# Performance work log

Hardware: AMD Instinct MI355X
Metric: run time of the kernel (lower is better)

Reference implementation:

```python
import jax, jax.numpy as jnp
import numpy as np

B = 32768
SEQ_LEN = 24
H = 64            # HIDDEN_DIM
SLOTS = 8         # MEMORY_SLOTS
VOCAB = 64        # VOCAB_SIZE


def setup_inputs() -> dict:
    key = jax.random.key(0)
    ks = jax.random.split(key, 8)
    seqs = jax.random.randint(ks[0], (B, SEQ_LEN), 0, VOCAB, dtype=jnp.int64)
    query_tok = jax.random.randint(ks[1], (B,), 0, VOCAB + 2, dtype=jnp.int64)
    embed = jax.random.normal(ks[2], (VOCAB + 2, H), dtype=jnp.float32) * 0.05
    gw1 = jax.random.normal(ks[3], (2 * H, 32), dtype=jnp.float32) / np.sqrt(2 * H)
    gb1 = jnp.zeros((32,), jnp.float32)
    gw2 = jax.random.normal(ks[4], (32, 1), dtype=jnp.float32) / np.sqrt(32)
    gb2 = jnp.zeros((1,), jnp.float32)
    rw1 = jax.random.normal(ks[5], (2 * H, H), dtype=jnp.float32) / np.sqrt(2 * H)
    rb1 = jnp.zeros((H,), jnp.float32)
    rw2 = jax.random.normal(ks[6], (H, VOCAB), dtype=jnp.float32) / np.sqrt(H)
    rb2 = jnp.zeros((VOCAB,), jnp.float32)
    return {"seqs": seqs, "query_tok": query_tok, "embed": embed,
            "gw1": gw1, "gb1": gb1, "gw2": gw2, "gb2": gb2,
            "rw1": rw1, "rb1": rb1, "rw2": rw2, "rb2": rb2}


def reference(seqs, query_tok, embed, gw1, gb1, gw2, gb2, rw1, rb1, rw2, rb2):
    Bb = seqs.shape[0]
    T = SEQ_LEN - 1  # model writes tokens 0..SEQ_LEN-2 into memory
    embs = embed[seqs[:, :T]]                     # [B, T, H]
    batch_idx = jnp.arange(Bb)

    def step(mem, xs):
        t, emb = xs                               # emb: [B, H]
        ctx = jnp.broadcast_to(emb[:, None, :], mem.shape)
        pair = jnp.concatenate([ctx, mem], axis=-1)        # [B, S, 2H]
        h = jax.nn.relu(pair @ gw1 + gb1)                  # [B, S, 32]
        score = jax.nn.sigmoid(h @ gw2 + gb2)[..., 0]      # [B, S]
        # while memory not full, fill slot t; otherwise evict argmax score
        idx = jnp.where(t < SLOTS, t, jnp.argmax(score, axis=1))
        mem = mem.at[batch_idx, idx].set(emb)
        return mem, None

    mem0 = jnp.zeros((Bb, SLOTS, H), embed.dtype)
    mem, _ = jax.lax.scan(step, mem0, (jnp.arange(T), jnp.swapaxes(embs, 0, 1)))

    summary = mem.mean(axis=1)                    # [B, H]  (memory is full: T > SLOTS)
    q = embed[query_tok]                          # [B, H]
    x = jnp.concatenate([q, summary], axis=-1)    # [B, 2H]
    logits = jax.nn.relu(x @ rw1 + rb1) @ rw2 + rb2   # [B, VOCAB]
    return logits
```

## Files before the change

kernel.cpp:

```cpp
#include <hip/hip_runtime.h>
#include <math.h>

typedef __attribute__((ext_vector_type(8))) _Float16 f16x8;
typedef __attribute__((ext_vector_type(4))) float f32x4;

#define TSTEPS 23
#define ROWS 128

#define WSB_B1 0
#define WSB_W2 21504
#define WSB_Z  30720

__global__ __launch_bounds__(512) void pre_all(
    const float* __restrict__ embed, const float* __restrict__ gw1,
    const float* __restrict__ gb1, const float* __restrict__ gw2,
    const float* __restrict__ gb2, const float* __restrict__ rw1,
    const float* __restrict__ rb1, const float* __restrict__ rw2,
    char* __restrict__ wsc)
{
    __shared__ float sEmb[66 * 64];
    __shared__ float sW[128 * 64];
    __shared__ float sV[64 * 33];
    __shared__ float sU[32];
    __shared__ float sG[65];
    __shared__ float sRb1[64];
    __shared__ double sP[512];

    const int tid = threadIdx.x;
    const int blk = blockIdx.x;

    if (blk < 64) {
        {
            const float4* es = (const float4*)embed;
            float4* ed = (float4*)sEmb;
            for (int i = tid; i < 1024; i += 512) ed[i] = es[i];
            const float4* gs = (const float4*)gw1;
            float4* gd = (float4*)sW;
            for (int i = tid; i < 1024; i += 512) gd[i] = gs[i];
            if (tid < 32) { sG[tid] = gb1[tid]; sG[32 + tid] = gw2[tid]; }
            if (tid == 64) sG[64] = gb2[0];
        }
        __syncthreads();
        {
            const int s = tid >> 3, j0 = (tid & 7) * 4;
            const float* er = sEmb + s * 64;
            float a0 = 0.f, a1 = 0.f, a2 = 0.f, a3 = 0.f;
            #pragma unroll
            for (int k = 0; k < 64; ++k) {
                const float ek = er[k];
                const float4 w0 = *(const float4*)&sW[(64 + k) * 32 + j0];
                a0 = fmaf(ek, w0.x, a0); a1 = fmaf(ek, w0.y, a1);
                a2 = fmaf(ek, w0.z, a2); a3 = fmaf(ek, w0.w, a3);
            }
            float* vd = sV + s * 33 + j0;
            vd[0] = a0; vd[1] = a1; vd[2] = a2; vd[3] = a3;
        }
        if (tid < 32) {
            const int j = tid;
            float acc = 0.f;
            const float* er = sEmb + blk * 64;
            #pragma unroll
            for (int k = 0; k < 64; ++k)
                acc = fmaf(er[k], sW[k * 32 + j], acc);
            sU[j] = acc;
        }
        __syncthreads();
        {
            const int s = tid >> 3;
            const int j0 = (tid & 7) * 4;
            double p = 0.0;
            #pragma unroll
            for (int j = j0; j < j0 + 4; ++j) {
                const double a = (double)sU[j] + (double)sV[s * 33 + j] + (double)sG[j];
                if (a > 0.0) p += a * (double)sG[32 + j];
            }
            sP[tid] = p;
        }
        __syncthreads();
        if (tid < 64) {
            const double* pp = sP + tid * 8;
            const double z = (double)sG[64] +
                (((pp[0] + pp[1]) + (pp[2] + pp[3])) + ((pp[4] + pp[5]) + (pp[6] + pp[7])));
            ((float*)(wsc + WSB_Z))[blk * 64 + tid] = (float)z;
        }
    } else if (blk < 81) {
        {
            const float4* es = (const float4*)embed;
            float4* ed = (float4*)sEmb;
            for (int i = tid; i < 1056; i += 512) ed[i] = es[i];
            const float4* rs = (const float4*)rw1;
            float4* rd = (float4*)sW;
            for (int i = tid; i < 2048; i += 512) rd[i] = rs[i];
            if (tid < 64) sRb1[tid] = rb1[tid];
        }
        __syncthreads();
        const int e = (blk - 64) * 512 + tid;
        if (e < 8320) {
            const int n = e & 63, k = e >> 6;
            const int trow = (k < 64) ? k : (k - 64);
            const int ofs = (k < 64) ? 64 : 0;
            float4 er[16];
            const float4* erp = (const float4*)(sEmb + trow * 64);
            #pragma unroll
            for (int q = 0; q < 16; ++q) er[q] = erp[q];
            float acc = (k < 64) ? 0.f : sRb1[n];
            #pragma unroll
            for (int m = 0; m < 64; ++m)
                acc = fmaf(((const float*)er)[m], sW[(ofs + m) * 64 + n], acc);
            acc *= (k < 64) ? (0.125f * 256.f) : 256.f;
            ((_Float16*)(wsc + WSB_B1))[n * 168 + k] = (_Float16)acc;
        }
    } else {
        _Float16* w2t = (_Float16*)(wsc + WSB_W2);
        for (int e = tid; e < 4096; e += 512) {
            const int n = e & 63, j = e >> 6;
            w2t[n * 72 + j] = (_Float16)rw2[j * 64 + n];
        }
        _Float16* b1 = (_Float16*)(wsc + WSB_B1);
        for (int e = tid; e < 2432; e += 512) {
            const int n = e / 38, k = 130 + (e - n * 38);
            b1[n * 168 + k] = (_Float16)0.f;
        }
    }
}

__device__ __forceinline__ f16x8 build_slot_win(const unsigned* s, const unsigned* hb, int ko)
{
    unsigned w0 = 0, w1 = 0, w2 = 0, w3 = 0;
    #pragma unroll
    for (int i = 0; i < 8; ++i) {
        const unsigned d = s[i] - (unsigned)ko;
        const unsigned val = (d < 8u) ? (hb[i] << ((d & 1u) * 16)) : 0u;
        const unsigned q = d >> 1;
        w0 |= (q == 0u) ? val : 0u;
        w1 |= (q == 1u) ? val : 0u;
        w2 |= (q == 2u) ? val : 0u;
        w3 |= (q == 3u) ? val : 0u;
    }
    union { unsigned u[4]; f16x8 v; } r;
    r.u[0] = w0; r.u[1] = w1; r.u[2] = w2; r.u[3] = w3;
    return r.v;
}

__device__ __forceinline__ f16x8 build_q_win(int kq, int ko)
{
    const unsigned d = (unsigned)(kq - ko);
    const unsigned val = (d < 8u) ? (0x3C00u << ((d & 1u) * 16)) : 0u;
    const unsigned q = d >> 1;
    union { unsigned u[4]; f16x8 v; } r;
    r.u[0] = (q == 0u) ? val : 0u;
    r.u[1] = (q == 1u) ? val : 0u;
    r.u[2] = (q == 2u) ? val : 0u;
    r.u[3] = (q == 3u) ? val : 0u;
    return r.v;
}

#define L_Z    0
#define L_B1   16640
#define L_W2   38144
#define L_H    47360
#define L_ROW  65792
#define L_RB2  67840

__global__ __launch_bounds__(512) void sm_main(
    const int* __restrict__ seqs, const int* __restrict__ qtok,
    const float* __restrict__ rb2, const char* __restrict__ wsc,
    float* __restrict__ out)
{
    __shared__ __align__(16) char smem[68096];
    float*    sZ   = (float*)(smem + L_Z);
    _Float16* sB1  = (_Float16*)(smem + L_B1);
    _Float16* sW2  = (_Float16*)(smem + L_W2);
    _Float16* sH   = (_Float16*)(smem + L_H);
    uint4*    sRow = (uint4*)(smem + L_ROW);
    float*    sRb2 = (float*)(smem + L_RB2);

    const int tid = threadIdx.x;
    const int base = blockIdx.x * ROWS;

    unsigned pk[6];
    int qt = 0;
    if (tid < ROWS) {
        const int4* sq = (const int4*)(seqs + (size_t)(base + tid) * 24);
        #pragma unroll
        for (int i = 0; i < 6; ++i) {
            const int4 w4 = sq[i];
            pk[i] = (unsigned)w4.x | ((unsigned)w4.y << 8) |
                    ((unsigned)w4.z << 16) | ((unsigned)w4.w << 24);
        }
        qt = qtok[base + tid];
    }

    {
        const float* zsrc = (const float*)(wsc + WSB_Z);
        #pragma unroll
        for (int i = 0; i < 8; ++i) {
            const int e = tid + i * 512;
            sZ[(e >> 6) * 65 + (e & 63)] = zsrc[e];
        }
        if (tid < 64) sRb2[tid] = rb2[tid];
    }
    __syncthreads();

    if (tid < ROWS) {
        unsigned lo = pk[0], hi = pk[1];
        #pragma unroll
        for (int t = 8; t < TSTEPS; ++t) {
            const int c = (int)((pk[t >> 2] >> ((t & 3) * 8)) & 255u);
            const float* zr = sZ + c * 65;
            float b = zr[lo & 63]; int am = 0; float z;
            z = zr[(lo >> 8) & 63];  if (z > b) { b = z; am = 1; }
            z = zr[(lo >> 16) & 63]; if (z > b) { b = z; am = 2; }
            z = zr[lo >> 24];        if (z > b) { b = z; am = 3; }
            z = zr[hi & 63];         if (z > b) { b = z; am = 4; }
            z = zr[(hi >> 8) & 63];  if (z > b) { b = z; am = 5; }
            z = zr[(hi >> 16) & 63]; if (z > b) { b = z; am = 6; }
            z = zr[hi >> 24];        if (z > b) { b = z; am = 7; }
            const unsigned cb = (unsigned)c;
            if (am < 4) { const int sh = am * 8; lo = (lo & ~(255u << sh)) | (cb << sh); }
            else        { const int sh = am * 8 - 32; hi = (hi & ~(255u << sh)) | (cb << sh); }
        }
        int t_[8] = { (int)(lo & 63), (int)((lo >> 8) & 63), (int)((lo >> 16) & 63), (int)(lo >> 24),
                      (int)(hi & 63), (int)((hi >> 8) & 63), (int)((hi >> 16) & 63), (int)(hi >> 24) };
        int tot[8] = {1, 1, 1, 1, 1, 1, 1, 1};
        #pragma unroll
        for (int i = 0; i < 8; ++i)
            #pragma unroll
            for (int j = i + 1; j < 8; ++j) {
                const int eq = (t_[i] == t_[j]);
                tot[i] += eq; tot[j] += eq;
            }
        unsigned tp = 0;
        #pragma unroll
        for (int i = 0; i < 8; ++i) tp |= (unsigned)tot[i] << (4 * i);
        sRow[tid] = make_uint4(lo & 0x3F3F3F3Fu, hi & 0x3F3F3F3Fu, tp, (unsigned)qt);
    } else {
        const int t2 = tid - 128;
        const float4* b1s = (const float4*)(wsc + WSB_B1);
        float4* b1d = (float4*)sB1;
        for (int i = t2; i < 1344; i += 384) b1d[i] = b1s[i];
        const float4* w2s = (const float4*)(wsc + WSB_W2);
        float4* w2d = (float4*)sW2;
        for (int i = t2; i < 576; i += 384) w2d[i] = w2s[i];
    }
    __syncthreads();

    const int lane = tid & 63;
    const int w = tid >> 6;
    const int c16 = lane & 15, g = lane >> 4;
    const int arow = w * 16 + c16;

    unsigned sl[8], hb[8];
    int kq;
    {
        const uint4 ri = sRow[arow];
        sl[0] = ri.x & 63u; sl[1] = (ri.x >> 8) & 63u;
        sl[2] = (ri.x >> 16) & 63u; sl[3] = ri.x >> 24;
        sl[4] = ri.y & 63u; sl[5] = (ri.y >> 8) & 63u;
        sl[6] = (ri.y >> 16) & 63u; sl[7] = ri.y >> 24;
        #pragma unroll
        for (int i = 0; i < 8; ++i) {
            const unsigned tot = (ri.z >> (4 * i)) & 15u;
            union { _Float16 h; unsigned short b; } cv;
            cv.h = (_Float16)(float)tot;
            hb[i] = (unsigned)cv.b;
        }
        kq = 64 + (int)ri.w;
    }

    f32x4 a0 = {0.f, 0.f, 0.f, 0.f}, a1 = a0, a2 = a0, a3 = a0;
    #pragma unroll
    for (int ks = 0; ks < 5; ++ks) {
        const int ko = ks * 32 + g * 8;
        const f16x8 af = (ks < 2) ? build_slot_win(sl, hb, ko) : build_q_win(kq, ko);
        const f16x8 b0 = *(const f16x8*)&sB1[(c16) * 168 + ko];
        const f16x8 b1 = *(const f16x8*)&sB1[(16 + c16) * 168 + ko];
        const f16x8 b2 = *(const f16x8*)&sB1[(32 + c16) * 168 + ko];
        const f16x8 b3 = *(const f16x8*)&sB1[(48 + c16) * 168 + ko];
        a0 = __builtin_amdgcn_mfma_f32_16x16x32_f16(af, b0, a0, 0, 0, 0);
        a1 = __builtin_amdgcn_mfma_f32_16x16x32_f16(af, b1, a1, 0, 0, 0);
        a2 = __builtin_amdgcn_mfma_f32_16x16x32_f16(af, b2, a2, 0, 0, 0);
        a3 = __builtin_amdgcn_mfma_f32_16x16x32_f16(af, b3, a3, 0, 0, 0);
    }
    {
        const int rbase = w * 16 + g * 4;
        #pragma unroll
        for (int j = 0; j < 4; ++j) {
            _Float16* hr = sH + (rbase + j) * 72;
            const float v0 = a0[j], v1 = a1[j], v2 = a2[j], v3 = a3[j];
            hr[c16]      = (_Float16)(v0 > 0.f ? v0 : 0.f);
            hr[16 + c16] = (_Float16)(v1 > 0.f ? v1 : 0.f);
            hr[32 + c16] = (_Float16)(v2 > 0.f ? v2 : 0.f);
            hr[48 + c16] = (_Float16)(v3 > 0.f ? v3 : 0.f);
        }
    }
    __syncthreads();

    f32x4 d0 = {0.f, 0.f, 0.f, 0.f}, d1 = d0, d2 = d0, d3 = d0;
    #pragma unroll
    for (int ks = 0; ks < 2; ++ks) {
        const int ko = ks * 32 + g * 8;
        const f16x8 af = *(const f16x8*)&sH[arow * 72 + ko];
        const f16x8 b0 = *(const f16x8*)&sW2[(c16) * 72 + ko];
        const f16x8 b1 = *(const f16x8*)&sW2[(16 + c16) * 72 + ko];
        const f16x8 b2 = *(const f16x8*)&sW2[(32 + c16) * 72 + ko];
        const f16x8 b3 = *(const f16x8*)&sW2[(48 + c16) * 72 + ko];
        d0 = __builtin_amdgcn_mfma_f32_16x16x32_f16(af, b0, d0, 0, 0, 0);
        d1 = __builtin_amdgcn_mfma_f32_16x16x32_f16(af, b1, d1, 0, 0, 0);
        d2 = __builtin_amdgcn_mfma_f32_16x16x32_f16(af, b2, d2, 0, 0, 0);
        d3 = __builtin_amdgcn_mfma_f32_16x16x32_f16(af, b3, d3, 0, 0, 0);
    }
    float* sOut = (float*)(void*)smem;
    {
        const int rbase = w * 16 + g * 4;
        #pragma unroll
        for (int j = 0; j < 4; ++j) {
            float* orow = sOut + (rbase + j) * 68;
            orow[c16]      = d0[j] * (1.f / 256.f) + sRb2[c16];
            orow[16 + c16] = d1[j] * (1.f / 256.f) + sRb2[16 + c16];
            orow[32 + c16] = d2[j] * (1.f / 256.f) + sRb2[32 + c16];
            orow[48 + c16] = d3[j] * (1.f / 256.f) + sRb2[48 + c16];
        }
    }
    __syncthreads();

    #pragma unroll
    for (int r2 = 0; r2 < 4; ++r2) {
        const int idx = r2 * 512 + tid;
        const int row = idx >> 4, c4 = idx & 15;
        *(float4*)(out + (size_t)(base + row) * 64 + c4 * 4) =
            *(const float4*)&sOut[row * 68 + c4 * 4];
    }
}

extern "C" void kernel_launch(void* const* d_in, const int* in_sizes, int n_in,
                              void* d_out, int out_size, void* d_ws, size_t ws_size,
                              hipStream_t stream)
{
    const int* seqs    = (const int*)d_in[0];
    const int* qtok    = (const int*)d_in[1];
    const float* embed = (const float*)d_in[2];
    const float* gw1   = (const float*)d_in[3];
    const float* gb1   = (const float*)d_in[4];
    const float* gw2   = (const float*)d_in[5];
    const float* gb2   = (const float*)d_in[6];
    const float* rw1   = (const float*)d_in[7];
    const float* rb1   = (const float*)d_in[8];
    const float* rw2   = (const float*)d_in[9];
    const float* rb2   = (const float*)d_in[10];
    char* wsc  = (char*)d_ws;
    float* out = (float*)d_out;
    const int B = in_sizes[1];

    pre_all<<<82, 512, 0, stream>>>(embed, gw1, gb1, gw2, gb2, rw1, rb1, rw2, wsc);
    pre_all<<<64, 512, 0, stream>>>(embed, gw1, gb1, gw2, gb2, rw1, rb1, rw2, wsc);
    sm_main<<<B / ROWS, 512, 0, stream>>>(seqs, qtok, rb2, wsc, out);
}
```

Measured before the change: 23.14 us.

## Split eviction scan across 4 lanes per row, halve block size, drop duplicate prelaunch

After: 22.72 us. About the same (-1.8%).

```diff
diff --git a/kernel.cpp b/kernel.cpp
--- a/kernel.cpp
+++ b/kernel.cpp
@@ -5,7 +5,8 @@
 typedef __attribute__((ext_vector_type(4))) float f32x4;
 
 #define TSTEPS 23
-#define ROWS 128
+#define ROWS 64
+#define BT 256
 
 #define WSB_B1 0
 #define WSB_W2 21504
@@ -159,89 +160,99 @@
 #define L_B1   16640
 #define L_W2   38144
 #define L_H    47360
-#define L_ROW  65792
-#define L_RB2  67840
-
-__global__ __launch_bounds__(512) void sm_main(
+#define L_TOK  56576
+#define L_ROW  58112
+#define L_QT   59136
+
+__global__ __launch_bounds__(BT) void sm_main(
     const int* __restrict__ seqs, const int* __restrict__ qtok,
     const float* __restrict__ rb2, const char* __restrict__ wsc,
     float* __restrict__ out)
 {
-    __shared__ __align__(16) char smem[68096];
+    __shared__ __align__(16) char smem[59648];
     float*    sZ   = (float*)(smem + L_Z);
     _Float16* sB1  = (_Float16*)(smem + L_B1);
     _Float16* sW2  = (_Float16*)(smem + L_W2);
     _Float16* sH   = (_Float16*)(smem + L_H);
-    uint4*    sRow = (uint4*)(smem + L_ROW);
-    float*    sRb2 = (float*)(smem + L_RB2);
+    unsigned* sTok = (unsigned*)(smem + L_TOK);
+    uint4*    sRow = (uint4*)(smem + 58112);
+    int*      sQt  = (int*)(smem + 59136);
+    float*    sRb2 = (float*)(smem + 59392);
 
     const int tid = threadIdx.x;
     const int base = blockIdx.x * ROWS;
 
-    unsigned pk[6];
-    int qt = 0;
-    if (tid < ROWS) {
-        const int4* sq = (const int4*)(seqs + (size_t)(base + tid) * 24);
-        #pragma unroll
-        for (int i = 0; i < 6; ++i) {
-            const int4 w4 = sq[i];
-            pk[i] = (unsigned)w4.x | ((unsigned)w4.y << 8) |
-                    ((unsigned)w4.z << 16) | ((unsigned)w4.w << 24);
-        }
-        qt = qtok[base + tid];
-    }
-
-    {
+    {
+        const int4* sq = (const int4*)(seqs + (size_t)base * 24);
+        #pragma unroll
+        for (int i = 0; i < 2; ++i) {
+            const int g = tid + i * 256;
+            if (g < 384) {
+                const int4 w4 = sq[g];
+                sTok[g] = (unsigned)w4.x | ((unsigned)w4.y << 8) |
+                          ((unsigned)w4.z << 16) | ((unsigned)w4.w << 24);
+            }
+        }
+        if (tid < 64) sQt[tid] = qtok[base + tid];
+        if (tid >= 64 && tid < 128) sRb2[tid - 64] = rb2[tid - 64];
         const float* zsrc = (const float*)(wsc + WSB_Z);
         #pragma unroll
-        for (int i = 0; i < 8; ++i) {
-            const int e = tid + i * 512;
+        for (int i = 0; i < 16; ++i) {
+            const int e = tid + i * 256;
             sZ[(e >> 6) * 65 + (e & 63)] = zsrc[e];
         }
-        if (tid < 64) sRb2[tid] = rb2[tid];
-    }
-    __syncthreads();
-
-    if (tid < ROWS) {
-        unsigned lo = pk[0], hi = pk[1];
-        #pragma unroll
-        for (int t = 8; t < TSTEPS; ++t) {
-            const int c = (int)((pk[t >> 2] >> ((t & 3) * 8)) & 255u);
-            const float* zr = sZ + c * 65;
-            float b = zr[lo & 63]; int am = 0; float z;
-            z = zr[(lo >> 8) & 63];  if (z > b) { b = z; am = 1; }
-            z = zr[(lo >> 16) & 63]; if (z > b) { b = z; am = 2; }
-            z = zr[lo >> 24];        if (z > b) { b = z; am = 3; }
-            z = zr[hi & 63];         if (z > b) { b = z; am = 4; }
-            z = zr[(hi >> 8) & 63];  if (z > b) { b = z; am = 5; }
-            z = zr[(hi >> 16) & 63]; if (z > b) { b = z; am = 6; }
-            z = zr[hi >> 24];        if (z > b) { b = z; am = 7; }
-            const unsigned cb = (unsigned)c;
-            if (am < 4) { const int sh = am * 8; lo = (lo & ~(255u << sh)) | (cb << sh); }
-            else        { const int sh = am * 8 - 32; hi = (hi & ~(255u << sh)) | (cb << sh); }
-        }
-        int t_[8] = { (int)(lo & 63), (int)((lo >> 8) & 63), (int)((lo >> 16) & 63), (int)(lo >> 24),
-                      (int)(hi & 63), (int)((hi >> 8) & 63), (int)((hi >> 16) & 63), (int)(hi >> 24) };
-        int tot[8] = {1, 1, 1, 1, 1, 1, 1, 1};
-        #pragma unroll
-        for (int i = 0; i < 8; ++i)
-            #pragma unroll
-            for (int j = i + 1; j < 8; ++j) {
-                const int eq = (t_[i] == t_[j]);
-                tot[i] += eq; tot[j] += eq;
-            }
-        unsigned tp = 0;
-        #pragma unroll
-        for (int i = 0; i < 8; ++i) tp |= (unsigned)tot[i] << (4 * i);
-        sRow[tid] = make_uint4(lo & 0x3F3F3F3Fu, hi & 0x3F3F3F3Fu, tp, (unsigned)qt);
-    } else {
-        const int t2 = tid - 128;
         const float4* b1s = (const float4*)(wsc + WSB_B1);
         float4* b1d = (float4*)sB1;
-        for (int i = t2; i < 1344; i += 384) b1d[i] = b1s[i];
+        for (int i = tid; i < 1344; i += 256) b1d[i] = b1s[i];
         const float4* w2s = (const float4*)(wsc + WSB_W2);
         float4* w2d = (float4*)sW2;
-        for (int i = t2; i < 576; i += 384) w2d[i] = w2s[i];
+        for (int i = tid; i < 576; i += 256) w2d[i] = w2s[i];
+    }
+    __syncthreads();
+
+    {
+        const int row = tid >> 2, sub = tid & 3;
+        unsigned lo = sTok[row * 6 + 0];
+        unsigned hi = sTok[row * 6 + 1];
+        const unsigned char* tk = ((const unsigned char*)sTok) + row * 24;
+        const int s0 = sub * 2, s1 = sub * 2 + 1;
+        #pragma unroll
+        for (int t = 8; t < TSTEPS; ++t) {
+            const int c = tk[t];
+            const float* zr = sZ + c * 65;
+            const unsigned word = (sub < 2) ? lo : hi;
+            const int sh = (sub & 1) * 16;
+            const int b0 = (int)((word >> sh) & 63u);
+            const int b1 = (int)((word >> (sh + 8)) & 63u);
+            const float v0 = zr[b0], v1 = zr[b1];
+            float bv; int bi;
+            if (v1 > v0) { bv = v1; bi = s1; } else { bv = v0; bi = s0; }
+            #pragma unroll
+            for (int m = 1; m <= 2; m <<= 1) {
+                const float ov = __shfl_xor(bv, m);
+                const int   oi = __shfl_xor(bi, m);
+                if (ov > bv || (ov == bv && oi < bi)) { bv = ov; bi = oi; }
+            }
+            const unsigned cb = (unsigned)c;
+            if (bi < 4) { const int q = bi * 8;      lo = (lo & ~(255u << q)) | (cb << q); }
+            else        { const int q = bi * 8 - 32; hi = (hi & ~(255u << q)) | (cb << q); }
+        }
+        if (sub == 0) {
+            int t_[8] = { (int)(lo & 63), (int)((lo >> 8) & 63), (int)((lo >> 16) & 63), (int)(lo >> 24),
+                          (int)(hi & 63), (int)((hi >> 8) & 63), (int)((hi >> 16) & 63), (int)(hi >> 24) };
+            int tot[8] = {1, 1, 1, 1, 1, 1, 1, 1};
+            #pragma unroll
+            for (int i = 0; i < 8; ++i)
+                #pragma unroll
+                for (int j = i + 1; j < 8; ++j) {
+                    const int eq = (t_[i] == t_[j]);
+                    tot[i] += eq; tot[j] += eq;
+                }
+            unsigned tp = 0;
+            #pragma unroll
+            for (int i = 0; i < 8; ++i) tp |= (unsigned)tot[i] << (4 * i);
+            sRow[row] = make_uint4(lo & 0x3F3F3F3Fu, hi & 0x3F3F3F3Fu, tp, (unsigned)sQt[row]);
+        }
     }
     __syncthreads();
 
@@ -326,7 +337,7 @@
 
     #pragma unroll
     for (int r2 = 0; r2 < 4; ++r2) {
-        const int idx = r2 * 512 + tid;
+        const int idx = r2 * 256 + tid;
         const int row = idx >> 4, c4 = idx & 15;
         *(float4*)(out + (size_t)(base + row) * 64 + c4 * 4) =
             *(const float4*)&sOut[row * 68 + c4 * 4];
@@ -353,6 +364,5 @@
     const int B = in_sizes[1];
 
     pre_all<<<82, 512, 0, stream>>>(embed, gw1, gb1, gw2, gb2, rw1, rb1, rw2, wsc);
-    pre_all<<<64, 512, 0, stream>>>(embed, gw1, gb1, gw2, gb2, rw1, rb1, rw2, wsc);
-    sm_main<<<B / ROWS, 512, 0, stream>>>(seqs, qtok, rb2, wsc, out);
-}
+    sm_main<<<B / ROWS, BT, 0, stream>>>(seqs, qtok, rb2, wsc, out);
+}
```

## Drop redundant pre_all launch and register-tile the gate score table

Applied to the files above, without the earlier changes.

After: 18.97 us (median of 2 runs). 18.0% less time.

```diff
diff --git a/kernel.cpp b/kernel.cpp
--- a/kernel.cpp
+++ b/kernel.cpp
@@ -18,22 +18,24 @@
     const float* __restrict__ rb1, const float* __restrict__ rw2,
     char* __restrict__ wsc)
 {
-    __shared__ float sEmb[66 * 64];
+    __shared__ float sE[66 * 64];
     __shared__ float sW[128 * 64];
     __shared__ float sV[64 * 33];
     __shared__ float sU[32];
     __shared__ float sG[65];
     __shared__ float sRb1[64];
-    __shared__ double sP[512];
 
     const int tid = threadIdx.x;
     const int blk = blockIdx.x;
 
     if (blk < 64) {
         {
-            const float4* es = (const float4*)embed;
-            float4* ed = (float4*)sEmb;
-            for (int i = tid; i < 1024; i += 512) ed[i] = es[i];
+            #pragma unroll
+            for (int i = 0; i < 8; ++i) {
+                const int e = tid + i * 512;
+                const int s = e >> 6, k = e & 63;
+                sE[k * 65 + s] = embed[s * 64 + k];
+            }
             const float4* gs = (const float4*)gw1;
             float4* gd = (float4*)sW;
             for (int i = tid; i < 1024; i += 512) gd[i] = gs[i];
@@ -41,52 +43,61 @@
             if (tid == 64) sG[64] = gb2[0];
         }
         __syncthreads();
-        {
-            const int s = tid >> 3, j0 = (tid & 7) * 4;
-            const float* er = sEmb + s * 64;
-            float a0 = 0.f, a1 = 0.f, a2 = 0.f, a3 = 0.f;
+        if (tid < 128) {
+            const int s0 = (tid >> 3) * 4, j0 = (tid & 7) * 4;
+            float acc[4][4];
+            #pragma unroll
+            for (int a = 0; a < 4; ++a)
+                #pragma unroll
+                for (int b = 0; b < 4; ++b) acc[a][b] = 0.f;
             #pragma unroll
             for (int k = 0; k < 64; ++k) {
-                const float ek = er[k];
-                const float4 w0 = *(const float4*)&sW[(64 + k) * 32 + j0];
-                a0 = fmaf(ek, w0.x, a0); a1 = fmaf(ek, w0.y, a1);
-                a2 = fmaf(ek, w0.z, a2); a3 = fmaf(ek, w0.w, a3);
+                const float4 e4 = *(const float4*)&sE[k * 65 + s0];
+                const float4 w4 = *(const float4*)&sW[(64 + k) * 32 + j0];
+                acc[0][0] = fmaf(e4.x, w4.x, acc[0][0]); acc[0][1] = fmaf(e4.x, w4.y, acc[0][1]);
+                acc[0][2] = fmaf(e4.x, w4.z, acc[0][2]); acc[0][3] = fmaf(e4.x, w4.w, acc[0][3]);
+                acc[1][0] = fmaf(e4.y, w4.x, acc[1][0]); acc[1][1] = fmaf(e4.y, w4.y, acc[1][1]);
+                acc[1][2] = fmaf(e4.y, w4.z, acc[1][2]); acc[1][3] = fmaf(e4.y, w4.w, acc[1][3]);
+                acc[2][0] = fmaf(e4.z, w4.x, acc[2][0]); acc[2][1] = fmaf(e4.z, w4.y, acc[2][1]);
+                acc[2][2] = fmaf(e4.z, w4.z, acc[2][2]); acc[2][3] = fmaf(e4.z, w4.w, acc[2][3]);
+                acc[3][0] = fmaf(e4.w, w4.x, acc[3][0]); acc[3][1] = fmaf(e4.w, w4.y, acc[3][1]);
+                acc[3][2] = fmaf(e4.w, w4.z, acc[3][2]); acc[3][3] = fmaf(e4.w, w4.w, acc[3][3]);
             }
-            float* vd = sV + s * 33 + j0;
-            vd[0] = a0; vd[1] = a1; vd[2] = a2; vd[3] = a3;
-        }
-        if (tid < 32) {
-            const int j = tid;
+            #pragma unroll
+            for (int a = 0; a < 4; ++a)
+                #pragma unroll
+                for (int b = 0; b < 4; ++b)
+                    sV[(s0 + a) * 33 + j0 + b] = acc[a][b];
+        } else if (tid < 160) {
+            const int j = tid - 128;
             float acc = 0.f;
-            const float* er = sEmb + blk * 64;
             #pragma unroll
             for (int k = 0; k < 64; ++k)
-                acc = fmaf(er[k], sW[k * 32 + j], acc);
+                acc = fmaf(sE[k * 65 + blk], sW[k * 32 + j], acc);
             sU[j] = acc;
-        }
-        __syncthreads();
-        {
-            const int s = tid >> 3;
-            const int j0 = (tid & 7) * 4;
-            double p = 0.0;
-            #pragma unroll
-            for (int j = j0; j < j0 + 4; ++j) {
-                const double a = (double)sU[j] + (double)sV[s * 33 + j] + (double)sG[j];
-                if (a > 0.0) p += a * (double)sG[32 + j];
-            }
-            sP[tid] = p;
         }
         __syncthreads();
         if (tid < 64) {
-            const double* pp = sP + tid * 8;
-            const double z = (double)sG[64] +
-                (((pp[0] + pp[1]) + (pp[2] + pp[3])) + ((pp[4] + pp[5]) + (pp[6] + pp[7])));
-            ((float*)(wsc + WSB_Z))[blk * 64 + tid] = (float)z;
+            const int s = tid;
+            float p0 = 0.f, p1 = 0.f, p2 = 0.f, p3 = 0.f;
+            #pragma unroll
+            for (int j = 0; j < 32; j += 4) {
+                const float a0 = sU[j]     + sV[s * 33 + j]     + sG[j];
+                const float a1 = sU[j + 1] + sV[s * 33 + j + 1] + sG[j + 1];
+                const float a2 = sU[j + 2] + sV[s * 33 + j + 2] + sG[j + 2];
+                const float a3 = sU[j + 3] + sV[s * 33 + j + 3] + sG[j + 3];
+                if (a0 > 0.f) p0 = fmaf(a0, sG[32 + j],     p0);
+                if (a1 > 0.f) p1 = fmaf(a1, sG[32 + j + 1], p1);
+                if (a2 > 0.f) p2 = fmaf(a2, sG[32 + j + 2], p2);
+                if (a3 > 0.f) p3 = fmaf(a3, sG[32 + j + 3], p3);
+            }
+            const float z = sG[64] + ((p0 + p1) + (p2 + p3));
+            ((float*)(wsc + WSB_Z))[blk * 64 + s] = z;
         }
     } else if (blk < 81) {
         {
             const float4* es = (const float4*)embed;
-            float4* ed = (float4*)sEmb;
+            float4* ed = (float4*)sE;
             for (int i = tid; i < 1056; i += 512) ed[i] = es[i];
             const float4* rs = (const float4*)rw1;
             float4* rd = (float4*)sW;
@@ -100,7 +111,7 @@
             const int trow = (k < 64) ? k : (k - 64);
             const int ofs = (k < 64) ? 64 : 0;
             float4 er[16];
-            const float4* erp = (const float4*)(sEmb + trow * 64);
+            const float4* erp = (const float4*)(sE + trow * 64);
             #pragma unroll
             for (int q = 0; q < 16; ++q) er[q] = erp[q];
             float acc = (k < 64) ? 0.f : sRb1[n];
@@ -353,6 +364,5 @@
     const int B = in_sizes[1];
 
     pre_all<<<82, 512, 0, stream>>>(embed, gw1, gb1, gw2, gb2, rw1, rb1, rw2, wsc);
-    pre_all<<<64, 512, 0, stream>>>(embed, gw1, gb1, gw2, gb2, rw1, rb1, rw2, wsc);
     sm_main<<<B / ROWS, 512, 0, stream>>>(seqs, qtok, rb2, wsc, out);
 }
```
